# Optimization experiments

Hardware: AMD Instinct MI355X
Metric: run time of the kernel (lower is better)

Reference implementation:

```python
import jax, jax.numpy as jnp
import numpy as np

HEADS = 4
DIM_HEAD = 32
SCALE = DIM_HEAD ** -0.5


def setup_inputs() -> dict:
    key = jax.random.key(0)
    ks = jax.random.split(key, 7)
    b, c, h, w = 2, 256, 64, 64
    time_dim = 512
    hidden = HEADS * DIM_HEAD  # 128
    return {
        "x": jax.random.normal(ks[0], (b, c, h, w), jnp.float32),
        "time_emb": jax.random.normal(ks[1], (b, time_dim), jnp.float32),
        "w_mlp": jax.random.normal(ks[2], (2 * c, time_dim), jnp.float32) * 0.02,
        "b_mlp": jax.random.normal(ks[3], (2 * c,), jnp.float32) * 0.02,
        "w_qkv": jax.random.normal(ks[4], (3 * hidden, c), jnp.float32) * 0.05,
        "w_out": jax.random.normal(ks[5], (c, hidden), jnp.float32) * 0.05,
        "b_out": jax.random.normal(ks[6], (c,), jnp.float32) * 0.02,
    }


def reference(x, time_emb, w_mlp, b_mlp, w_qkv, w_out, b_out):
    b, c, h, w = x.shape
    n = h * w
    # FiLM conditioning: SiLU -> Linear -> chunk into (scale, shift)
    t = jax.nn.silu(time_emb) @ w_mlp.T + b_mlp            # [b, 2c]
    scale, shift = jnp.split(t, 2, axis=1)                  # [b, c] each
    x = x * (scale + 1.0)[:, :, None, None] + shift[:, :, None, None]
    # 1x1 conv QKV projection (no bias)
    qkv = jnp.einsum('oc,bchw->bohw', w_qkv, x)             # [b, 3*hidden, h, w]
    q, k, v = jnp.split(qkv, 3, axis=1)                     # [b, hidden, h, w]
    def to_heads(t):
        return t.reshape(b, HEADS, DIM_HEAD, n)             # b h d (x y)
    q, k, v = to_heads(q) * SCALE, to_heads(k), to_heads(v)
    sim = jnp.einsum('bhdi,bhdj->bhij', q, k)               # [b, h, n, n]
    attn = jax.nn.softmax(sim, axis=-1)
    out = jnp.einsum('bhij,bhdj->bhid', attn, v)            # [b, h, n, d]
    # b h (x y) d -> b (h d) x y
    out = out.transpose(0, 1, 3, 2).reshape(b, HEADS * DIM_HEAD, h, w)
    return jnp.einsum('oc,bchw->bohw', w_out, out) + b_out[None, :, None, None]
```

## Files before the change

### kernel.cpp

```cpp
#include <hip/hip_runtime.h>


typedef __bf16 bf16x8 __attribute__((ext_vector_type(8)));
typedef float  f32x16 __attribute__((ext_vector_type(16)));
typedef unsigned uint2v __attribute__((ext_vector_type(2)));

#define MFMA(a, b, c) __builtin_amdgcn_mfma_f32_32x32x16_bf16((a), (b), (c), 0, 0, 0)
#define PLSWAP(a, b) __builtin_amdgcn_permlane32_swap((a), (b), false, false)

static constexpr float kLOG2E = 1.4426950408889634f;
static constexpr float kSCALE = 0.17677669529663687f;

__device__ __forceinline__ unsigned short bf16r(float x) {
  union { float f; unsigned u; } v; v.f = x;
  return (unsigned short)((v.u + 0x7FFFu + ((v.u >> 16) & 1u)) >> 16);
}
__device__ __forceinline__ float fast_silu(float x) {
  return x / (1.0f + __builtin_amdgcn_exp2f(-x * kLOG2E));
}
__device__ __forceinline__ f32x16 zero16() {
  f32x16 z;
#pragma unroll
  for (int i = 0; i < 16; ++i) z[i] = 0.0f;
  return z;
}
__device__ __forceinline__ bf16x8 ld_frag(const unsigned short* p) {
  return *reinterpret_cast<const bf16x8*>(p);
}

__global__ __launch_bounds__(256) void prep(const float* __restrict__ x,
                                            unsigned short* __restrict__ xT,
                                            const float* __restrict__ te,
                                            const float* __restrict__ w_mlp,
                                            const float* __restrict__ b_mlp,
                                            float* __restrict__ fparams) {
  __shared__ unsigned short lds[64][66];
  int bid = blockIdx.x;
  if (bid < 32) {
    int g = bid * 256 + threadIdx.x;
    int pair = g >> 3, ks = g & 7;
    int b = pair >> 9, o = pair & 511;
    const float4* w4 = (const float4*)(w_mlp + (size_t)o * 512 + ks * 64);
    const float4* t4 = (const float4*)(te + (size_t)b * 512 + ks * 64);
    float s = 0.0f;
#pragma unroll 4
    for (int k = 0; k < 16; ++k) {
      float4 wv = w4[k];
      float4 tv = t4[k];
      s += wv.x * fast_silu(tv.x) + wv.y * fast_silu(tv.y) +
           wv.z * fast_silu(tv.z) + wv.w * fast_silu(tv.w);
    }
    s += __shfl_xor(s, 1, 64);
    s += __shfl_xor(s, 2, 64);
    s += __shfl_xor(s, 4, 64);
    if (ks == 0) {
      float t_val = s + b_mlp[o];
      fparams[b * 512 + o] = (o < 256) ? (t_val + 1.0f) : t_val;
    }
    return;
  }
  int bid2 = bid - 32;
  int p0 = (bid2 & 63) * 64;
  int c0 = ((bid2 >> 6) & 3) * 64;
  int b  = bid2 >> 8;
  int t = threadIdx.x;
  int pl = t & 63, cw = t >> 6;
  const float* xb = x + ((size_t)b * 256 + c0) * 4096 + p0;
#pragma unroll
  for (int r = 0; r < 16; ++r) {
    int cl = cw + r * 4;
    lds[pl][cl] = bf16r(xb[(size_t)cl * 4096 + pl]);
  }
  __syncthreads();
  unsigned short* out = xT + ((size_t)b * 4096 + p0) * 256 + c0;
#pragma unroll
  for (int rep = 0; rep < 2; ++rep) {
    int ch = t + rep * 256;
    int pr = ch >> 3, cc = (ch & 7) * 8;
    union { unsigned short u[8]; uint4 v; } pk;
#pragma unroll
    for (int i = 0; i < 8; ++i) pk.u[i] = lds[pr][cc + i];
    *(uint4*)(out + (size_t)pr * 256 + cc) = pk.v;
  }
}

__global__ __launch_bounds__(256) void film2(const float* __restrict__ w_qkv,
                                             const float* __restrict__ fparams,
                                             const float* __restrict__ w_out,
                                             unsigned short* __restrict__ Aeff,
                                             float* __restrict__ qb,
                                             unsigned short* __restrict__ WoBf) {
  int tid = blockIdx.x * 256 + threadIdx.x;
  if (tid < 24576) {
    int row = tid >> 5, cs = tid & 31;
    int b = row / 384, o = row % 384;
    float qs = (o < 128) ? (kSCALE * kLOG2E) : 1.0f;
    const float4* wr  = (const float4*)(w_qkv + (size_t)o * 256);
    const float4* sc4 = (const float4*)(fparams + b * 512);
    const float4* sh4 = (const float4*)(fparams + b * 512 + 256);
    unsigned short* arow = Aeff + ((size_t)b * 384 + o) * 256;
    float acc = 0.0f;
#pragma unroll
    for (int j = 0; j < 2; ++j) {
      int c4 = cs * 2 + j;
      float4 wv = wr[c4], scv = sc4[c4], shv = sh4[c4];
      acc += wv.x * shv.x + wv.y * shv.y + wv.z * shv.z + wv.w * shv.w;
      union { unsigned short u[4]; unsigned long long q; } pk;
      pk.u[0] = bf16r(wv.x * scv.x * qs);
      pk.u[1] = bf16r(wv.y * scv.y * qs);
      pk.u[2] = bf16r(wv.z * scv.z * qs);
      pk.u[3] = bf16r(wv.w * scv.w * qs);
      *(unsigned long long*)(arow + c4 * 4) = pk.q;
    }
    acc += __shfl_xor(acc, 1, 64);
    acc += __shfl_xor(acc, 2, 64);
    acc += __shfl_xor(acc, 4, 64);
    acc += __shfl_xor(acc, 8, 64);
    acc += __shfl_xor(acc, 16, 64);
    if (cs == 0) qb[b * 384 + o] = acc * qs;
  } else {
    int t = tid - 24576;
    const float4* src = (const float4*)(w_out + (size_t)t * 64);
    unsigned short* dst = WoBf + (size_t)t * 64;
#pragma unroll 4
    for (int i = 0; i < 16; ++i) {
      float4 v = src[i];
      union { unsigned short u[4]; unsigned long long q; } pk;
      pk.u[0] = bf16r(v.x); pk.u[1] = bf16r(v.y);
      pk.u[2] = bf16r(v.z); pk.u[3] = bf16r(v.w);
      *(unsigned long long*)(dst + i * 4) = pk.q;
    }
  }
}

__global__ __launch_bounds__(64) void qkv_gemm(const unsigned short* __restrict__ Aeff,
                                               const float* __restrict__ qb,
                                               const unsigned short* __restrict__ xT,
                                               unsigned short* __restrict__ Qb,
                                               unsigned short* __restrict__ Kb,
                                               unsigned short* __restrict__ Vt) {
  int bid = blockIdx.x;
  int o_blk = bid % 12;
  int rest = bid / 12;
  int b = rest & 1, p_blk = rest >> 1;
  int l = threadIdx.x, col = l & 31, hi = l >> 5;

  const unsigned short* Ab = Aeff + ((size_t)b * 384 + o_blk * 32) * 256;
  const unsigned short* Bb = xT + ((size_t)b * 4096 + p_blk * 32) * 256;

  f32x16 acc = zero16();
#pragma unroll
  for (int kc = 0; kc < 256; kc += 16) {
    bf16x8 a0 = ld_frag(Ab + (size_t)col * 256 + kc + hi * 8);
    bf16x8 b0 = ld_frag(Bb + (size_t)col * 256 + kc + hi * 8);
    acc = MFMA(a0, b0, acc);
  }

  int obase = o_blk * 32;
  int sec = obase >> 7;
  int head = (obase & 127) >> 5;
  size_t bh = (size_t)b * 4 + head;
  int p = p_blk * 32 + col;
  if (sec < 2) {
    unsigned short* dst = (sec == 0 ? Qb : Kb) + (bh * 4096 + p) * 32;
#pragma unroll
    for (int g = 0; g < 4; ++g) {
      int dbase = 8 * g + 4 * hi;
      union { unsigned short u[4]; unsigned long long q; } pk;
#pragma unroll
      for (int r = 0; r < 4; ++r)
        pk.u[r] = bf16r(acc[4 * g + r] + qb[b * 384 + obase + dbase + r]);
      *(unsigned long long*)(dst + dbase) = pk.q;
    }
  } else {
    unsigned short* dst = Vt + bh * 32 * 4096;
#pragma unroll
    for (int reg = 0; reg < 16; ++reg) {
      int d = (reg & 3) + 8 * (reg >> 2) + 4 * hi;
      dst[(size_t)d * 4096 + p] = bf16r(acc[reg] + qb[b * 384 + obase + d]);
    }
  }
}

__device__ __forceinline__ void softmax_pv(f32x16 S, bf16x8 va0, bf16x8 va1,
                                           f32x16& O, float& lsum) {
#pragma unroll
  for (int i = 0; i < 16; ++i) S[i] = __builtin_amdgcn_exp2f(S[i]);
  float s0 = (S[0] + S[1]) + (S[2] + S[3]);
  float s1 = (S[4] + S[5]) + (S[6] + S[7]);
  float s2 = (S[8] + S[9]) + (S[10] + S[11]);
  float s3 = (S[12] + S[13]) + (S[14] + S[15]);
  lsum += (s0 + s1) + (s2 + s3);
  union { __bf16 h[16]; unsigned u[8]; } pu;
#pragma unroll
  for (int i = 0; i < 16; ++i) pu.h[i] = (__bf16)S[i];
  uint2v r0 = PLSWAP(pu.u[0], pu.u[2]);
  uint2v r1 = PLSWAP(pu.u[1], pu.u[3]);
  uint2v r2 = PLSWAP(pu.u[4], pu.u[6]);
  uint2v r3 = PLSWAP(pu.u[5], pu.u[7]);
  union { unsigned u[4]; bf16x8 v; } B0, B1;
  B0.u[0] = r0[0]; B0.u[1] = r1[0]; B0.u[2] = r0[1]; B0.u[3] = r1[1];
  B1.u[0] = r2[0]; B1.u[1] = r3[0]; B1.u[2] = r2[1]; B1.u[3] = r3[1];
  O = MFMA(va0, B0.v, O);
  O = MFMA(va1, B1.v, O);
}

__global__ __launch_bounds__(512, 4) void attn(const unsigned short* __restrict__ Qb,
                                               const unsigned short* __restrict__ Kb,
                                               const unsigned short* __restrict__ Vt,
                                               unsigned short* __restrict__ Ob) {
  __shared__ float Olds[8][2][16][64];
  __shared__ float llds[8][2][64];

  int bid = blockIdx.x;
  int bh = bid >> 6;
  int q0 = (bid & 63) * 64;
  int w = threadIdx.x >> 6;
  int l = threadIdx.x & 63, col = l & 31, hi = l >> 5;

  const unsigned short* Qp = Qb + ((size_t)bh * 4096 + q0) * 32;
  bf16x8 qf0 = ld_frag(Qp + col * 32 + hi * 8);
  bf16x8 qf1 = ld_frag(Qp + col * 32 + 16 + hi * 8);
  bf16x8 qg0 = ld_frag(Qp + (col + 32) * 32 + hi * 8);
  bf16x8 qg1 = ld_frag(Qp + (col + 32) * 32 + 16 + hi * 8);

  const unsigned short* kp =
      Kb + (size_t)bh * 131072 + (size_t)(w * 512 + col) * 32 + hi * 8;
  const unsigned short* vp =
      Vt + (size_t)bh * 131072 + (size_t)col * 4096 + w * 512 + hi * 8;

  const f32x16 zc = zero16();
  f32x16 Oa = zero16(), Obb = zero16();
  float lsuma = 0.0f, lsumb = 0.0f;

  for (int it = 0; it < 16; ++it) {
    bf16x8 ka0 = ld_frag(kp);
    bf16x8 ka1 = ld_frag(kp + 16);
    bf16x8 va0 = ld_frag(vp);
    bf16x8 va1 = ld_frag(vp + 16);
    kp += 1024; vp += 32;

    f32x16 Sa = MFMA(ka0, qf0, zc);
    Sa = MFMA(ka1, qf1, Sa);
    softmax_pv(Sa, va0, va1, Oa, lsuma);

    f32x16 Sb = MFMA(ka0, qg0, zc);
    Sb = MFMA(ka1, qg1, Sb);
    softmax_pv(Sb, va0, va1, Obb, lsumb);
  }

  uint2v lra = PLSWAP(__float_as_uint(lsuma), __float_as_uint(lsuma));
  uint2v lrb = PLSWAP(__float_as_uint(lsumb), __float_as_uint(lsumb));
  float lta = __uint_as_float(lra[0]) + __uint_as_float(lra[1]);
  float ltb = __uint_as_float(lrb[0]) + __uint_as_float(lrb[1]);

#pragma unroll
  for (int i = 0; i < 16; ++i) {
    Olds[w][0][i][l] = Oa[i];
    Olds[w][1][i][l] = Obb[i];
  }
  llds[w][0][l] = lta;
  llds[w][1][l] = ltb;
  __syncthreads();

  int reg0 = 2 * w;
  int based = 8 * (w >> 1) + 2 * (w & 1) + 4 * hi;
#pragma unroll
  for (int h = 0; h < 2; ++h) {
    float L = ((llds[0][h][l] + llds[1][h][l]) + (llds[2][h][l] + llds[3][h][l])) +
              ((llds[4][h][l] + llds[5][h][l]) + (llds[6][h][l] + llds[7][h][l]));
    float inv = 1.0f / L;
    float v0 = 0.0f, v1 = 0.0f;
#pragma unroll
    for (int i = 0; i < 8; ++i) {
      v0 += Olds[i][h][reg0][l];
      v1 += Olds[i][h][reg0 + 1][l];
    }
    unsigned short* dst =
        Ob + ((size_t)bh * 4096 + q0 + h * 32 + col) * 32 + based;
    union { unsigned short u[2]; unsigned q; } pk2;
    pk2.u[0] = bf16r(v0 * inv);
    pk2.u[1] = bf16r(v1 * inv);
    *(unsigned*)dst = pk2.q;
  }
}

__global__ __launch_bounds__(64) void out_gemm(const unsigned short* __restrict__ Wo,
                                               const unsigned short* __restrict__ Ob,
                                               const float* __restrict__ b_out,
                                               float* __restrict__ out) {
  int bid = blockIdx.x;
  int o_blk = bid & 7;
  int rest = bid >> 3;
  int b = rest & 1, p_blk = rest >> 1;
  int l = threadIdx.x, col = l & 31, hi = l >> 5;

  const unsigned short* Ab = Wo + (size_t)(o_blk * 32) * 128;
  f32x16 acc = zero16();
#pragma unroll
  for (int kc = 0; kc < 128; kc += 16) {
    int head = kc >> 5;
    int doff = (kc & 16) + hi * 8;
    const unsigned short* Bb =
        Ob + (((size_t)b * 4 + head) * 4096 + p_blk * 32) * 32 + doff;
    bf16x8 a0 = ld_frag(Ab + (size_t)col * 128 + kc + hi * 8);
    bf16x8 b0 = ld_frag(Bb + (size_t)col * 32);
    acc = MFMA(a0, b0, acc);
  }
  int p = p_blk * 32 + col;
#pragma unroll
  for (int reg = 0; reg < 16; ++reg) {
    int o = o_blk * 32 + (reg & 3) + 8 * (reg >> 2) + 4 * hi;
    out[((size_t)b * 256 + o) * 4096 + p] = acc[reg] + b_out[o];
  }
}

extern "C" void kernel_launch(void* const* d_in, const int* in_sizes, int n_in,
                              void* d_out, int out_size, void* d_ws, size_t ws_size,
                              hipStream_t stream) {
  const float* x     = (const float*)d_in[0];
  const float* te    = (const float*)d_in[1];
  const float* w_mlp = (const float*)d_in[2];
  const float* b_mlp = (const float*)d_in[3];
  const float* w_qkv = (const float*)d_in[4];
  const float* w_out = (const float*)d_in[5];
  const float* b_out = (const float*)d_in[6];

  char* ws = (char*)d_ws;
  float*          fparams = (float*)(ws + 0);
  float*          qb      = (float*)(ws + 4096);
  unsigned short* Aeff    = (unsigned short*)(ws + 8192);
  unsigned short* WoBf    = (unsigned short*)(ws + 401408);
  unsigned short* xT      = (unsigned short*)(ws + 466944);
  unsigned short* Qb      = (unsigned short*)(ws + 4661248);
  unsigned short* Kb      = (unsigned short*)(ws + 6758400);
  unsigned short* Vt      = (unsigned short*)(ws + 8855552);
  unsigned short* Ob      = (unsigned short*)(ws + 10952704);
  float* out = (float*)d_out;

  hipLaunchKernelGGL(prep, dim3(544), dim3(256), 0, stream, x, xT, te, w_mlp,
                     b_mlp, fparams);
  hipLaunchKernelGGL(film2, dim3(98), dim3(256), 0, stream, w_qkv, fparams, w_out,
                     Aeff, qb, WoBf);
  hipLaunchKernelGGL(qkv_gemm, dim3(3072), dim3(64), 0, stream, Aeff, qb, xT, Qb, Kb, Vt);
  hipLaunchKernelGGL(attn, dim3(512), dim3(512), 0, stream, Qb, Kb, Vt, Ob);
  hipLaunchKernelGGL(out_gemm, dim3(2048), dim3(64), 0, stream, WoBf, Ob, b_out, out);
}
```

Baseline: 134.9 us.

## Split attention over keys with LDS-staged K/V tiles and separate merge kernel

The attention kernel now splits the key range into 8 chunks across blocks. Each 4-wave block stages a shared 32-key K/V tile in double-buffered LDS, where previously every wave streamed K/V from global memory on its own. To make each tile contiguous, V is stored tiled per 32-position block. Partial fp32 outputs and row sums go to global memory and are combined by a new merge kernel, replacing the in-block LDS reduction. This cuts redundant K/V global/L2 traffic, but adds a large fp32 partial-result round trip, two barriers per iteration and an extra launch.

```diff
diff --git a/kernel.cpp b/kernel.cpp
--- a/kernel.cpp
+++ b/kernel.cpp
@@ -26,6 +26,12 @@
 }
 __device__ __forceinline__ bf16x8 ld_frag(const unsigned short* p) {
   return *reinterpret_cast<const bf16x8*>(p);
+}
+__device__ __forceinline__ bf16x8 ld_lds_frag(const unsigned short* p) {
+  union { unsigned long long q[2]; bf16x8 v; } u;
+  u.q[0] = *(const unsigned long long*)(p);
+  u.q[1] = *(const unsigned long long*)(p + 4);
+  return u.v;
 }
 
 __global__ __launch_bounds__(256) void prep(const float* __restrict__ x,
@@ -173,11 +179,11 @@
       *(unsigned long long*)(dst + dbase) = pk.q;
     }
   } else {
-    unsigned short* dst = Vt + bh * 32 * 4096;
+    unsigned short* dst = Vt + bh * 131072 + (size_t)p_blk * 1024;
 #pragma unroll
     for (int reg = 0; reg < 16; ++reg) {
       int d = (reg & 3) + 8 * (reg >> 2) + 4 * hi;
-      dst[(size_t)d * 4096 + p] = bf16r(acc[reg] + qb[b * 384 + obase + d]);
+      dst[d * 32 + col] = bf16r(acc[reg] + qb[b * 384 + obase + d]);
     }
   }
 }
@@ -205,40 +211,50 @@
   O = MFMA(va1, B1.v, O);
 }
 
-__global__ __launch_bounds__(512, 4) void attn(const unsigned short* __restrict__ Qb,
+__global__ __launch_bounds__(256, 4) void attn(const unsigned short* __restrict__ Qb,
                                                const unsigned short* __restrict__ Kb,
                                                const unsigned short* __restrict__ Vt,
-                                               unsigned short* __restrict__ Ob) {
-  __shared__ float Olds[8][2][16][64];
-  __shared__ float llds[8][2][64];
+                                               float* __restrict__ Opart,
+                                               float* __restrict__ Lpart) {
+  __shared__ unsigned short kv[2][2][32][36];
 
   int bid = blockIdx.x;
-  int bh = bid >> 6;
-  int q0 = (bid & 63) * 64;
-  int w = threadIdx.x >> 6;
-  int l = threadIdx.x & 63, col = l & 31, hi = l >> 5;
-
+  int qblk = bid & 15;
+  int ks   = (bid >> 4) & 7;
+  int bh   = bid >> 7;
+  int t = threadIdx.x;
+  int w = t >> 6, l = t & 63, col = l & 31, hi = l >> 5;
+
+  int q0 = qblk * 256 + w * 64;
   const unsigned short* Qp = Qb + ((size_t)bh * 4096 + q0) * 32;
   bf16x8 qf0 = ld_frag(Qp + col * 32 + hi * 8);
   bf16x8 qf1 = ld_frag(Qp + col * 32 + 16 + hi * 8);
   bf16x8 qg0 = ld_frag(Qp + (col + 32) * 32 + hi * 8);
   bf16x8 qg1 = ld_frag(Qp + (col + 32) * 32 + 16 + hi * 8);
 
-  const unsigned short* kp =
-      Kb + (size_t)bh * 131072 + (size_t)(w * 512 + col) * 32 + hi * 8;
-  const unsigned short* vp =
-      Vt + (size_t)bh * 131072 + (size_t)col * 4096 + w * 512 + hi * 8;
+  int sec = t >> 7, rr = (t & 127) >> 2, cc = t & 3;
+  const unsigned short* gsrc =
+      (sec ? Vt : Kb) + (size_t)bh * 131072 + ks * 16384 + (t & 127) * 8;
 
   const f32x16 zc = zero16();
   f32x16 Oa = zero16(), Obb = zero16();
   float lsuma = 0.0f, lsumb = 0.0f;
 
-  for (int it = 0; it < 16; ++it) {
-    bf16x8 ka0 = ld_frag(kp);
-    bf16x8 ka1 = ld_frag(kp + 16);
-    bf16x8 va0 = ld_frag(vp);
-    bf16x8 va1 = ld_frag(vp + 16);
-    kp += 1024; vp += 32;
+  uint4 greg = *(const uint4*)(gsrc);
+
+  for (int tt = 0; tt < 16; ++tt) {
+    __syncthreads();
+    int buf = tt & 1;
+    unsigned short* d0 = &kv[buf][sec][rr][cc * 8];
+    *(unsigned long long*)(d0)     = ((const unsigned long long*)&greg)[0];
+    *(unsigned long long*)(d0 + 4) = ((const unsigned long long*)&greg)[1];
+    if (tt < 15) greg = *(const uint4*)(gsrc + (tt + 1) * 1024);
+    __syncthreads();
+
+    bf16x8 ka0 = ld_lds_frag(&kv[buf][0][col][hi * 8]);
+    bf16x8 ka1 = ld_lds_frag(&kv[buf][0][col][16 + hi * 8]);
+    bf16x8 va0 = ld_lds_frag(&kv[buf][1][col][hi * 8]);
+    bf16x8 va1 = ld_lds_frag(&kv[buf][1][col][16 + hi * 8]);
 
     f32x16 Sa = MFMA(ka0, qf0, zc);
     Sa = MFMA(ka1, qf1, Sa);
@@ -254,35 +270,40 @@
   float lta = __uint_as_float(lra[0]) + __uint_as_float(lra[1]);
   float ltb = __uint_as_float(lrb[0]) + __uint_as_float(lrb[1]);
 
-#pragma unroll
-  for (int i = 0; i < 16; ++i) {
-    Olds[w][0][i][l] = Oa[i];
-    Olds[w][1][i][l] = Obb[i];
-  }
-  llds[w][0][l] = lta;
-  llds[w][1][l] = ltb;
-  __syncthreads();
-
-  int reg0 = 2 * w;
-  int based = 8 * (w >> 1) + 2 * (w & 1) + 4 * hi;
-#pragma unroll
-  for (int h = 0; h < 2; ++h) {
-    float L = ((llds[0][h][l] + llds[1][h][l]) + (llds[2][h][l] + llds[3][h][l])) +
-              ((llds[4][h][l] + llds[5][h][l]) + (llds[6][h][l] + llds[7][h][l]));
-    float inv = 1.0f / L;
-    float v0 = 0.0f, v1 = 0.0f;
-#pragma unroll
-    for (int i = 0; i < 8; ++i) {
-      v0 += Olds[i][h][reg0][l];
-      v1 += Olds[i][h][reg0 + 1][l];
-    }
-    unsigned short* dst =
-        Ob + ((size_t)bh * 4096 + q0 + h * 32 + col) * 32 + based;
-    union { unsigned short u[2]; unsigned q; } pk2;
-    pk2.u[0] = bf16r(v0 * inv);
-    pk2.u[1] = bf16r(v1 * inv);
-    *(unsigned*)dst = pk2.q;
-  }
+  float* op = Opart + (size_t)(bh * 8 + ks) * 131072;
+  float* lp = Lpart + (size_t)(bh * 8 + ks) * 4096;
+#pragma unroll
+  for (int r = 0; r < 16; ++r) {
+    int d = (r & 3) + 8 * (r >> 2) + 4 * hi;
+    op[d * 4096 + q0 + col]      = Oa[r];
+    op[d * 4096 + q0 + 32 + col] = Obb[r];
+  }
+  if (hi == 0) {
+    lp[q0 + col]      = lta;
+    lp[q0 + 32 + col] = ltb;
+  }
+}
+
+__global__ __launch_bounds__(256) void attn_merge(const float* __restrict__ Opart,
+                                                  const float* __restrict__ Lpart,
+                                                  unsigned short* __restrict__ Ob) {
+  int idx = blockIdx.x * 256 + threadIdx.x;
+  int dp = idx & 15;
+  int q  = (idx >> 4) & 4095;
+  int bh = idx >> 16;
+  float s0 = 0.0f, s1 = 0.0f, L = 0.0f;
+#pragma unroll
+  for (int ks = 0; ks < 8; ++ks) {
+    const float* op = Opart + (size_t)(bh * 8 + ks) * 131072;
+    s0 += op[(2 * dp) * 4096 + q];
+    s1 += op[(2 * dp + 1) * 4096 + q];
+    L  += Lpart[(size_t)(bh * 8 + ks) * 4096 + q];
+  }
+  float inv = 1.0f / L;
+  union { unsigned short u[2]; unsigned v; } pk;
+  pk.u[0] = bf16r(s0 * inv);
+  pk.u[1] = bf16r(s1 * inv);
+  *(unsigned*)(Ob + ((size_t)bh * 4096 + q) * 32 + 2 * dp) = pk.v;
 }
 
 __global__ __launch_bounds__(64) void out_gemm(const unsigned short* __restrict__ Wo,
@@ -336,6 +357,8 @@
   unsigned short* Kb      = (unsigned short*)(ws + 6758400);
   unsigned short* Vt      = (unsigned short*)(ws + 8855552);
   unsigned short* Ob      = (unsigned short*)(ws + 10952704);
+  float*          Opart   = (float*)(ws + 13049856);
+  float*          Lpart   = (float*)(ws + 46604288);
   float* out = (float*)d_out;
 
   hipLaunchKernelGGL(prep, dim3(544), dim3(256), 0, stream, x, xT, te, w_mlp,
@@ -343,6 +366,7 @@
   hipLaunchKernelGGL(film2, dim3(98), dim3(256), 0, stream, w_qkv, fparams, w_out,
                      Aeff, qb, WoBf);
   hipLaunchKernelGGL(qkv_gemm, dim3(3072), dim3(64), 0, stream, Aeff, qb, xT, Qb, Kb, Vt);
-  hipLaunchKernelGGL(attn, dim3(512), dim3(512), 0, stream, Qb, Kb, Vt, Ob);
+  hipLaunchKernelGGL(attn, dim3(1024), dim3(256), 0, stream, Qb, Kb, Vt, Opart, Lpart);
+  hipLaunchKernelGGL(attn_merge, dim3(2048), dim3(256), 0, stream, Opart, Lpart, Ob);
   hipLaunchKernelGGL(out_gemm, dim3(2048), dim3(64), 0, stream, WoBf, Ob, b_out, out);
 }
```

Result: slower. 148.7 us (+10.2%).
